# Kernel tuning notes

Measured on AMD Instinct MI355X. Metric: run time of the kernel, lower is better.

## Reference

```python
import jax, jax.numpy as jnp
import numpy as np

B, S, D, I, L, H, F = 4, 512, 768, 64, 2, 12, 3072
DH = D // H
LN_EPS = 1e-12


def setup_inputs() -> dict:
    key = jax.random.key(0)
    ks = jax.random.split(key, 24)
    nrm = lambda k, sh, s=0.02: jax.random.normal(k, sh, jnp.float32) * s
    return {
        'hs0': nrm(ks[0], (B, S, D), 1.0),
        'hs1': nrm(ks[1], (B, S, D), 1.0),
        'hs2': nrm(ks[2], (B, S, D), 1.0),
        'Wq': nrm(ks[3], (L, D, D)), 'bq': jnp.zeros((L, D), jnp.float32),
        'Wk': nrm(ks[4], (L, D, D)), 'bk': jnp.zeros((L, D), jnp.float32),
        'Wv': nrm(ks[5], (L, D, D)), 'bv': jnp.zeros((L, D), jnp.float32),
        'Wo': nrm(ks[6], (L, D, D)), 'bo': jnp.zeros((L, D), jnp.float32),
        'ln1_g': jnp.ones((L, D), jnp.float32), 'ln1_b': jnp.zeros((L, D), jnp.float32),
        'W1': nrm(ks[7], (L, D, F)), 'b1': jnp.zeros((L, F), jnp.float32),
        'W2': nrm(ks[8], (L, F, D)), 'b2': jnp.zeros((L, D), jnp.float32),
        'ln2_g': jnp.ones((L, D), jnp.float32), 'ln2_b': jnp.zeros((L, D), jnp.float32),
        'zero_context': nrm(ks[9], (D,), 1.0),
        'ck2tok_mask': jax.random.uniform(ks[10], (B, I, S)) > 0.7,  # True = token excluded from span
        'span_size_ids': jax.random.randint(ks[11], (B, I), 0, 10),
    }


def _ln(x, g, b):
    m = jnp.mean(x, axis=-1, keepdims=True)
    v = jnp.mean((x - m) ** 2, axis=-1, keepdims=True)
    return (x - m) * jax.lax.rsqrt(v + LN_EPS) * g + b


def _forward(hs0, hs1, Wq, bq, Wk, bk, Wv, bv, Wo, bo, ln1_g, ln1_b,
             W1, b1, W2, b2, ln2_g, ln2_b, zero_context, mask):
    # mask: [B,I,S] bool, True = excluded token
    zero_indic = jnp.all(mask, axis=-1)                 # [B,I] spans with no valid token
    mask = mask & ~zero_indic[:, :, None]               # unmask degenerate rows (replaced at end)
    # masked max pooling (init aggregation) -- [B,I,S,D] intermediate, traffic-bound
    pooled = jnp.max(jnp.where(mask[..., None], -jnp.inf, hs0[:, None, :, :]), axis=2)  # [B,I,D]
    ext = (mask.astype(jnp.float32) * -10000.0)[:, None, :, :]  # [B,1,I,S] extended attn mask
    q = pooled
    hs_list = (hs0, hs1)
    inv_sqrt_dh = np.float32(1.0 / np.sqrt(DH))
    for i in range(L):
        hs = hs_list[i]
        qh = (q @ Wq[i] + bq[i]).reshape(B, I, H, DH).transpose(0, 2, 1, 3)   # [B,H,I,DH]
        kh = (hs @ Wk[i] + bk[i]).reshape(B, S, H, DH).transpose(0, 2, 1, 3)  # [B,H,S,DH]
        vh = (hs @ Wv[i] + bv[i]).reshape(B, S, H, DH).transpose(0, 2, 1, 3)
        scores = jnp.einsum('bhid,bhsd->bhis', qh, kh) * inv_sqrt_dh + ext
        attn = jax.nn.softmax(scores, axis=-1)
        ctx = jnp.einsum('bhis,bhsd->bhid', attn, vh).transpose(0, 2, 1, 3).reshape(B, I, D)
        q = _ln(q + ctx @ Wo[i] + bo[i], ln1_g[i], ln1_b[i])
        ffn = jax.nn.gelu(q @ W1[i] + b1[i], approximate=False) @ W2[i] + b2[i]
        q = _ln(q + ffn, ln2_g[i], ln2_b[i])
    # zero-context substitution for empty spans
    return jnp.where(zero_indic[..., None], zero_context, q)


def reference(hs0, hs1, hs2, Wq, bq, Wk, bk, Wv, bv, Wo, bo, ln1_g, ln1_b,
              W1, b1, W2, b2, ln2_g, ln2_b, zero_context, ck2tok_mask, span_size_ids):
    # hs2 is the last entry of the (num_layers+1) slice; query layers 0..L-1 attend hs0..hs1.
    # span_size_ids unused since use_init_size_emb=False.
    del hs2, span_size_ids
    return _forward(hs0, hs1, Wq, bq, Wk, bk, Wv, bv, Wo, bo, ln1_g, ln1_b,
                    W1, b1, W2, b2, ln2_g, ln2_b, zero_context, ck2tok_mask)
```

## Files before the change

kernel.cpp:

```cpp
#include <hip/hip_runtime.h>
#include <hip/hip_bf16.h>
#include <math.h>

#define BB 4
#define SS 512
#define DD 768
#define II 64
#define LL 2
#define HH 12
#define FF 3072

using short8 = __attribute__((ext_vector_type(8))) short;
using f32x4  = __attribute__((ext_vector_type(4))) float;

__device__ __forceinline__ unsigned short f2bf(float x) {
  return __builtin_bit_cast(unsigned short, __float2bfloat16(x));
}

__device__ __forceinline__ void gload_lds16(const void* g, void* l) {
  __builtin_amdgcn_global_load_lds((const __attribute__((address_space(1))) unsigned int*)g,
                                   (__attribute__((address_space(3))) unsigned int*)l, 16, 0, 0);
}

struct TC { const float* s[6]; };

__global__ __launch_bounds__(256) void prep_kernel(
    TC src, unsigned short* __restrict__ WT4, unsigned short* __restrict__ W1T,
    unsigned short* __restrict__ W2T,
    const float* __restrict__ hs0, const float* __restrict__ hs1,
    unsigned short* __restrict__ hsb0, unsigned short* __restrict__ hsb1,
    const int* __restrict__ mask, int* __restrict__ zi, float* __restrict__ qf,
    unsigned short* __restrict__ qb, unsigned long long* __restrict__ pmask) {
  __shared__ float smem[4096];
  int id = blockIdx.x;
  int t = threadIdx.x;
  if (id < 3456) {
    const float* Ws; unsigned short* WTs; int K, N, k0, n0;
    if (id < 1152) {
      int z = id / 144, rem = id - z * 144;
      int widx = z >> 1, l = z & 1;
      Ws = src.s[widx] + (size_t)l * DD * DD;
      WTs = WT4 + ((size_t)widx * 2 + l) * DD * DD;
      K = DD; N = DD; k0 = (rem / 6) * 32; n0 = (rem % 6) * 128;
    } else if (id < 2304) {
      int j = id - 1152, l = j / 576, rem = j - l * 576;
      Ws = src.s[4] + (size_t)l * DD * FF;
      WTs = W1T + (size_t)l * FF * DD;
      K = DD; N = FF; k0 = (rem / 24) * 32; n0 = (rem % 24) * 128;
    } else {
      int j = id - 2304, l = j / 576, rem = j - l * 576;
      Ws = src.s[5] + (size_t)l * FF * DD;
      WTs = W2T + (size_t)l * DD * FF;
      K = FF; N = DD; k0 = (rem / 6) * 32; n0 = (rem % 6) * 128;
    }
    int w = t >> 6, lane = t & 63;
    #pragma unroll
    for (int cc = 0; cc < 4; ++cc) {
      int c = w * 4 + cc;
      int row = c * 2 + (lane >> 5);
      int cbyte = (lane & 31) * 16;
      int scb = cbyte ^ ((row & 7) << 4);
      gload_lds16((const char*)(Ws + (size_t)(k0 + row) * N + n0) + scb,
                  (char*)smem + c * 1024);
    }
    __syncthreads();
    int n = t >> 1, h2 = t & 1;
    union { unsigned short u[16]; uint4 v4[2]; } pk;
    #pragma unroll
    for (int i = 0; i < 16; ++i) {
      int kl = h2 * 16 + i;
      float f = *(const float*)((const char*)smem + kl * 512 + ((n * 4) ^ ((kl & 7) << 4)));
      pk.u[i] = f2bf(f);
    }
    uint4* dst = (uint4*)(WTs + (size_t)(n0 + n) * K + k0 + h2 * 16);
    dst[0] = pk.v4[0];
    dst[1] = pk.v4[1];
  } else if (id < 4992) {
    int idx = (id - 3456) * 256 + t;
    float4 va = ((const float4*)hs0)[idx];
    float4 vb = ((const float4*)hs1)[idx];
    union { unsigned short u[4]; uint2 v; } pa, pb;
    pa.u[0] = f2bf(va.x); pa.u[1] = f2bf(va.y); pa.u[2] = f2bf(va.z); pa.u[3] = f2bf(va.w);
    pb.u[0] = f2bf(vb.x); pb.u[1] = f2bf(vb.y); pb.u[2] = f2bf(vb.z); pb.u[3] = f2bf(vb.w);
    ((uint2*)hsb0)[idx] = pa.v;
    ((uint2*)hsb1)[idx] = pb.v;
  } else {
    float* eadd = smem;
    int j = id - 4992;
    int bi = j & 255, dz = j >> 8;
    int b = bi >> 6, w = t >> 6;
    const int* mrow = mask + (size_t)bi * SS;
    int m0v = mrow[t], m1v = mrow[t + 256];
    eadd[t] = m0v ? -__builtin_inff() : 0.0f;
    eadd[t + 256] = m1v ? -__builtin_inff() : 0.0f;
    int incl = (m0v == 0) | (m1v == 0);
    int any = __syncthreads_or(incl);
    int z = !any;
    if (dz == 0) {
      unsigned long long w0 = __ballot(z || (m0v == 0));
      unsigned long long w1 = __ballot(z || (m1v == 0));
      if ((t & 63) == 0) {
        pmask[bi * 8 + w] = w0;
        pmask[bi * 8 + 4 + w] = w1;
        if (t == 0) zi[bi] = z;
      }
    }
    const float* hb = hs0 + (size_t)b * SS * DD + dz * 256 + t;
    float m[8];
    #pragma unroll
    for (int jj = 0; jj < 8; ++jj) m[jj] = -3.4e38f;
    for (int s0 = 0; s0 < SS; s0 += 8) {
      #pragma unroll
      for (int jj = 0; jj < 8; ++jj)
        m[jj] = fmaxf(m[jj], hb[(size_t)(s0 + jj) * DD] + eadd[s0 + jj]);
    }
    float mm = fmaxf(fmaxf(fmaxf(m[0], m[1]), fmaxf(m[2], m[3])),
                     fmaxf(fmaxf(m[4], m[5]), fmaxf(m[6], m[7])));
    size_t o = (size_t)bi * DD + dz * 256 + t;
    qf[o] = mm;
    qb[o] = f2bf(mm);
  }
}

struct GB { const unsigned short* A; const unsigned short* Bt; const float* bias; void* C;
            int M; int N; int rowbias; };

template <int GELU, int OUTBF>
__global__ __launch_bounds__(256) void gemm_nt(GB g0, GB g1, GB g2, GB g3, int K) {
  __shared__ unsigned short Al[2][128 * 64];
  __shared__ unsigned short Bl[2][128 * 64];
  GB g = (blockIdx.z == 0) ? g0 : (blockIdx.z == 1) ? g1 : (blockIdx.z == 2) ? g2 : g3;
  int bm = blockIdx.x, bn = blockIdx.y;
  if (blockIdx.z & 1) { bm = blockIdx.y; bn = blockIdx.x; }
  if (bm * 128 >= g.M) return;
  int t = threadIdx.x, w = t >> 6, lane = t & 63;
  int hi = lane >> 4, lo = lane & 15;
  int wr = w >> 1, wc = w & 1;
  f32x4 acc[4][4] = {};
  const char* Abase = (const char*)g.A + (size_t)(bm * 128) * (size_t)K * 2;
  const char* Bbase = (const char*)g.Bt + (size_t)(bn * 128) * (size_t)K * 2;
  int rowbytes = K * 2;
  int KT = K >> 6;
  auto STAGE = [&](int buf, int kt) {
    int k0b = kt * 128;
    #pragma unroll
    for (int c = 0; c < 4; ++c) {
      int base = (c * 4 + w) << 10;
      int o = base + lane * 16;
      int row = o >> 7, cb = o & 127;
      int scb = cb ^ ((row & 7) << 4);
      gload_lds16(Abase + (size_t)row * rowbytes + (k0b + scb), (char*)Al[buf] + base);
      gload_lds16(Bbase + (size_t)row * rowbytes + (k0b + scb), (char*)Bl[buf] + base);
    }
  };
  STAGE(0, 0);
  asm volatile("s_waitcnt vmcnt(0)" ::: "memory");
  __builtin_amdgcn_s_barrier();
  int cur = 0;
  for (int kt = 0; kt < KT; ++kt) {
    if (kt + 1 < KT) STAGE(cur ^ 1, kt + 1);
    #pragma unroll
    for (int kk = 0; kk < 2; ++kk) {
      short8 av[4], bv_[4];
      #pragma unroll
      for (int mi = 0; mi < 4; ++mi) {
        int r = wr * 64 + mi * 16 + lo;
        av[mi] = *(const short8*)((const char*)Al[cur] + r * 128 + ((kk * 64 + hi * 16) ^ ((r & 7) << 4)));
      }
      #pragma unroll
      for (int ni = 0; ni < 4; ++ni) {
        int r = wc * 64 + ni * 16 + lo;
        bv_[ni] = *(const short8*)((const char*)Bl[cur] + r * 128 + ((kk * 64 + hi * 16) ^ ((r & 7) << 4)));
      }
      #pragma unroll
      for (int mi = 0; mi < 4; ++mi)
        #pragma unroll
        for (int ni = 0; ni < 4; ++ni)
          acc[mi][ni] = __builtin_amdgcn_mfma_f32_16x16x32_bf16(av[mi], bv_[ni], acc[mi][ni], 0, 0, 0);
    }
    if (kt + 1 < KT) {
      asm volatile("s_waitcnt vmcnt(0)" ::: "memory");
      __builtin_amdgcn_s_barrier();
      cur ^= 1;
    }
  }
  int mbase = bm * 128 + wr * 64;
  int nbase = bn * 128 + wc * 64;
  #pragma unroll
  for (int mi = 0; mi < 4; ++mi)
    #pragma unroll
    for (int ni = 0; ni < 4; ++ni)
      #pragma unroll
      for (int r = 0; r < 4; ++r) {
        int gm = mbase + mi * 16 + hi * 4 + r;
        int gn = nbase + ni * 16 + lo;
        float v = acc[mi][ni][r] + (g.rowbias ? g.bias[gm] : g.bias[gn]);
        if (GELU) v = 0.5f * v * (1.0f + erff(v * 0.70710678118654752f));
        if (OUTBF) ((unsigned short*)g.C)[(size_t)gm * g.N + gn] = f2bf(v);
        else       ((float*)g.C)[(size_t)gm * g.N + gn] = v;
      }
}

template <int GELU, int OUTBF, int PARTIAL>
__global__ __launch_bounds__(256) void gemm_sk(GB g, int K, int kLen) {
  __shared__ unsigned short Al[2][64 * 64];
  __shared__ unsigned short Bl[2][64 * 64];
  int bm = blockIdx.x, bn = blockIdx.y, bz = blockIdx.z;
  int t = threadIdx.x, w = t >> 6, lane = t & 63;
  int hi = lane >> 4, lo = lane & 15;
  int wr = w >> 1, wc = w & 1;
  f32x4 acc[2][2] = {};
  size_t rb = (size_t)K * 2;
  const char* Abase = (const char*)g.A + (size_t)(bm * 64) * rb + (size_t)bz * kLen * 2;
  const char* Bbase = (const char*)g.Bt + (size_t)(bn * 64) * rb + (size_t)bz * kLen * 2;
  int KT = kLen >> 6;
  auto STAGE = [&](int buf, int kt) {
    int k0b = kt * 128;
    #pragma unroll
    for (int c = 0; c < 2; ++c) {
      int base = (c * 4 + w) << 10;
      int o = base + lane * 16;
      int row = o >> 7, cb = o & 127;
      int scb = cb ^ ((row & 7) << 4);
      gload_lds16(Abase + (size_t)row * rb + (k0b + scb), (char*)Al[buf] + base);
      gload_lds16(Bbase + (size_t)row * rb + (k0b + scb), (char*)Bl[buf] + base);
    }
  };
  STAGE(0, 0);
  asm volatile("s_waitcnt vmcnt(0)" ::: "memory");
  __builtin_amdgcn_s_barrier();
  int cur = 0;
  for (int kt = 0; kt < KT; ++kt) {
    if (kt + 1 < KT) STAGE(cur ^ 1, kt + 1);
    #pragma unroll
    for (int kk = 0; kk < 2; ++kk) {
      short8 av[2], bv_[2];
      #pragma unroll
      for (int mi = 0; mi < 2; ++mi) {
        int r = wr * 32 + mi * 16 + lo;
        av[mi] = *(const short8*)((const char*)Al[cur] + r * 128 + ((kk * 64 + hi * 16) ^ ((r & 7) << 4)));
      }
      #pragma unroll
      for (int ni = 0; ni < 2; ++ni) {
        int r = wc * 32 + ni * 16 + lo;
        bv_[ni] = *(const short8*)((const char*)Bl[cur] + r * 128 + ((kk * 64 + hi * 16) ^ ((r & 7) << 4)));
      }
      #pragma unroll
      for (int mi = 0; mi < 2; ++mi)
        #pragma unroll
        for (int ni = 0; ni < 2; ++ni)
          acc[mi][ni] = __builtin_amdgcn_mfma_f32_16x16x32_bf16(av[mi], bv_[ni], acc[mi][ni], 0, 0, 0);
    }
    if (kt + 1 < KT) {
      asm volatile("s_waitcnt vmcnt(0)" ::: "memory");
      __builtin_amdgcn_s_barrier();
      cur ^= 1;
    }
  }
  int mbase = bm * 64 + wr * 32;
  int nbase = bn * 64 + wc * 32;
  #pragma unroll
  for (int mi = 0; mi < 2; ++mi)
    #pragma unroll
    for (int ni = 0; ni < 2; ++ni)
      #pragma unroll
      for (int r = 0; r < 4; ++r) {
        int gm = mbase + mi * 16 + hi * 4 + r;
        int gn = nbase + ni * 16 + lo;
        if (PARTIAL) {
          ((float*)g.C)[((size_t)bz * g.M + gm) * g.N + gn] = acc[mi][ni][r];
        } else {
          float v = acc[mi][ni][r] + g.bias[gn];
          if (GELU) v = 0.5f * v * (1.0f + erff(v * 0.70710678118654752f));
          if (OUTBF) ((unsigned short*)g.C)[(size_t)gm * g.N + gn] = f2bf(v);
          else       ((float*)g.C)[(size_t)gm * g.N + gn] = v;
        }
      }
}

#define ATTN_LDS 145664
__global__ __launch_bounds__(256) void attn_kernel(
    const unsigned short* __restrict__ qbuf, const unsigned short* __restrict__ WqTl,
    const float* __restrict__ bql, const unsigned short* __restrict__ khb,
    const unsigned short* __restrict__ vTall, const unsigned long long* __restrict__ pmask,
    unsigned short* __restrict__ ctx) {
  extern __shared__ char lds[];
  char* Qd = lds;
  char* KP = lds + 8192;
  char* Vd = lds + 8192 + 65536;
  unsigned long long* pm = (unsigned long long*)(lds + 139264);
  float* red  = (float*)(lds + 143360);
  float* red2 = (float*)(lds + 144384);
  float* rnv  = (float*)(lds + 145408);
  int bh = blockIdx.x;
  int b = bh / HH, h = bh - b * HH;
  int t = threadIdx.x, w = t >> 6, l = t & 63, hi = l >> 4, lo = l & 15;
  int o16 = l * 16, ro = o16 >> 7, cb = o16 & 127;

  const char* vsrc = (const char*)vTall + (size_t)(h * 64) * 4096 + (size_t)b * 1024;
  #pragma unroll
  for (int rr = 0; rr < 16; ++rr) {
    int rv = w * 16 + rr;
    gload_lds16(vsrc + (size_t)rv * 4096 + ((l * 16) ^ ((rv & 7) << 4)), Vd + rv * 1024);
  }
  if (w == 0) {
    const char* psrc = (const char*)pmask + (size_t)b * 4096;
    #pragma unroll
    for (int c = 0; c < 4; ++c) gload_lds16(psrc + c * 1024 + l * 16, (char*)pm + c * 1024);
  }

  const char* Aq = (const char*)qbuf + (size_t)(b * II) * 1536;
  const char* Bq = (const char*)WqTl + (size_t)(h * 64) * 1536;
  f32x4 qacc[4] = {};
  #pragma unroll
  for (int cc = 0; cc < 2; ++cc) {
    int ch = w * 2 + cc, row = ch * 8 + ro;
    int scb = cb ^ ((row & 7) << 4);
    gload_lds16(Aq + (size_t)row * 1536 + scb, KP + ch * 1024);
    gload_lds16(Bq + (size_t)row * 1536 + scb, KP + 8192 + ch * 1024);
  }
  __syncthreads();
  for (int kt = 0; kt < 12; ++kt) {
    int cur = (kt & 1) * 16384;
    if (kt < 11) {
      int nxt = ((kt + 1) & 1) * 16384;
      int kb = (kt + 1) * 128;
      #pragma unroll
      for (int cc = 0; cc < 2; ++cc) {
        int ch = w * 2 + cc, row = ch * 8 + ro;
        int scb = kb + (cb ^ ((row & 7) << 4));
        gload_lds16(Aq + (size_t)row * 1536 + scb, KP + nxt + ch * 1024);
        gload_lds16(Bq + (size_t)row * 1536 + scb, KP + nxt + 8192 + ch * 1024);
      }
    }
    #pragma unroll
    for (int kk = 0; kk < 2; ++kk) {
      int ra = w * 16 + lo;
      short8 av = *(const short8*)(KP + cur + ra * 128 + ((kk * 64 + hi * 16) ^ ((ra & 7) << 4)));
      #pragma unroll
      for (int ni = 0; ni < 4; ++ni) {
        int rb2 = ni * 16 + lo;
        short8 bv = *(const short8*)(KP + cur + 8192 + rb2 * 128 + ((kk * 64 + hi * 16) ^ ((rb2 & 7) << 4)));
        qacc[ni] = __builtin_amdgcn_mfma_f32_16x16x32_bf16(av, bv, qacc[ni], 0, 0, 0);
      }
    }
    __syncthreads();
  }
  #pragma unroll
  for (int ni = 0; ni < 4; ++ni)
    #pragma unroll
    for (int r = 0; r < 4; ++r) {
      int row = w * 16 + hi * 4 + r, col = ni * 16 + lo;
      float v = qacc[ni][r] + bql[h * 64 + col];
      *(unsigned short*)(Qd + row * 128 + ((col * 2) ^ ((row & 7) << 4))) = f2bf(v);
    }
  const char* Ks = (const char*)khb + (size_t)(b * SS) * 1536 + h * 128;
  #pragma unroll
  for (int cc = 0; cc < 16; ++cc) {
    int ch = w * 16 + cc, row = ch * 8 + ro;
    int scb = cb ^ ((row & 7) << 4);
    gload_lds16(Ks + (size_t)row * 1536 + scb, KP + ch * 1024);
  }
  __syncthreads();

  f32x4 acc[4][8] = {};
  #pragma unroll
  for (int kk = 0; kk < 2; ++kk) {
    short8 av[4];
    #pragma unroll
    for (int mi = 0; mi < 4; ++mi) {
      int ra = mi * 16 + lo;
      av[mi] = *(const short8*)(Qd + ra * 128 + ((kk * 64 + hi * 16) ^ ((ra & 7) << 4)));
    }
    #pragma unroll
    for (int ni = 0; ni < 8; ++ni) {
      int rk = w * 128 + ni * 16 + lo;
      short8 bv = *(const short8*)(KP + rk * 128 + ((kk * 64 + hi * 16) ^ ((rk & 7) << 4)));
      #pragma unroll
      for (int mi = 0; mi < 4; ++mi)
        acc[mi][ni] = __builtin_amdgcn_mfma_f32_16x16x32_bf16(av[mi], bv, acc[mi][ni], 0, 0, 0);
    }
  }
  #pragma unroll
  for (int mi = 0; mi < 4; ++mi)
    #pragma unroll
    for (int r = 0; r < 4; ++r) {
      float m = acc[mi][0][r];
      #pragma unroll
      for (int ni = 1; ni < 8; ++ni) m = fmaxf(m, acc[mi][ni][r]);
      #pragma unroll
      for (int xm = 1; xm <= 8; xm <<= 1) m = fmaxf(m, __shfl_xor(m, xm));
      if (lo == 0) red[(mi * 16 + hi * 4 + r) * 4 + w] = m;
    }
  __syncthreads();
  #pragma unroll
  for (int mi = 0; mi < 4; ++mi)
    #pragma unroll
    for (int r = 0; r < 4; ++r) {
      int row = mi * 16 + hi * 4 + r;
      float4 rm4 = *(const float4*)&red[row * 4];
      float gm = fmaxf(fmaxf(rm4.x, rm4.y), fmaxf(rm4.z, rm4.w));
      unsigned long long w0 = pm[row * 8 + w * 2 + 0];
      unsigned long long w1 = pm[row * 8 + w * 2 + 1];
      float s = 0.f;
      #pragma unroll
      for (int ni = 0; ni < 8; ++ni) {
        int sl = ni * 16 + lo;
        unsigned long long word = (sl < 64) ? w0 : w1;
        float in = ((word >> (sl & 63)) & 1ull) ? 1.0f : 0.0f;
        float e = __expf((acc[mi][ni][r] - gm) * 0.125f) * in;
        s += e;
        int sbyte = w * 256 + ni * 32 + lo * 2;
        *(unsigned short*)(KP + row * 1024 + (sbyte ^ ((row & 7) << 4))) = f2bf(e);
      }
      #pragma unroll
      for (int xm = 1; xm <= 8; xm <<= 1) s += __shfl_xor(s, xm);
      if (lo == 0) red2[row * 4 + w] = s;
    }
  __syncthreads();
  if (w == 0 && lo == 0) {
    #pragma unroll
    for (int mi = 0; mi < 4; ++mi)
      #pragma unroll
      for (int r = 0; r < 4; ++r) {
        int row = mi * 16 + hi * 4 + r;
        float4 s4 = *(const float4*)&red2[row * 4];
        rnv[row] = 1.0f / ((s4.x + s4.y) + (s4.z + s4.w));
      }
  }
  __syncthreads();
  f32x4 pacc[4] = {};
  for (int kk = 0; kk < 16; ++kk) {
    int rv = w * 16 + lo;
    short8 bv = *(const short8*)(Vd + rv * 1024 + ((kk * 64 + hi * 16) ^ ((rv & 7) << 4)));
    #pragma unroll
    for (int mi = 0; mi < 4; ++mi) {
      int ra = mi * 16 + lo;
      short8 av = *(const short8*)(KP + ra * 1024 + ((kk * 64 + hi * 16) ^ ((ra & 7) << 4)));
      pacc[mi] = __builtin_amdgcn_mfma_f32_16x16x32_bf16(av, bv, pacc[mi], 0, 0, 0);
    }
  }
  #pragma unroll
  for (int mi = 0; mi < 4; ++mi)
    #pragma unroll
    for (int r = 0; r < 4; ++r) {
      int row = mi * 16 + hi * 4 + r;
      ctx[(size_t)(b * II + row) * DD + h * 64 + w * 16 + lo] = f2bf(pacc[mi][r] * rnv[row]);
    }
}

template <int FINAL, int NP>
__global__ __launch_bounds__(256) void ln_kernel(const float* __restrict__ x, const float* __restrict__ y,
                                                 const float* __restrict__ gb,
                                                 const float* __restrict__ g, const float* __restrict__ bb,
                                                 float* __restrict__ qf, unsigned short* __restrict__ qb,
                                                 const int* __restrict__ zi, const float* __restrict__ zc,
                                                 float* __restrict__ out) {
  __shared__ float r1[4], r2[4];
  const int MN = BB * II * DD;
  int r = blockIdx.x, t = threadIdx.x;
  size_t o = (size_t)r * DD;
  float v0 = x[o + t] + gb[t];
  float v1 = x[o + t + 256] + gb[t + 256];
  float v2 = x[o + t + 512] + gb[t + 512];
  #pragma unroll
  for (int p = 0; p < NP; ++p) {
    size_t po = (size_t)p * MN + o;
    v0 += y[po + t];
    v1 += y[po + t + 256];
    v2 += y[po + t + 512];
  }
  float s = v0 + v1 + v2, ss = v0 * v0 + v1 * v1 + v2 * v2;
  #pragma unroll
  for (int o2 = 32; o2; o2 >>= 1) { s += __shfl_xor(s, o2); ss += __shfl_xor(ss, o2); }
  if ((t & 63) == 0) { r1[t >> 6] = s; r2[t >> 6] = ss; }
  __syncthreads();
  s = r1[0] + r1[1] + r1[2] + r1[3];
  ss = r2[0] + r2[1] + r2[2] + r2[3];
  float mean = s * (1.0f / DD);
  float var = ss * (1.0f / DD) - mean * mean;
  float inv = rsqrtf(var + 1e-12f);
  float w0 = (v0 - mean) * inv * g[t] + bb[t];
  float w1 = (v1 - mean) * inv * g[t + 256] + bb[t + 256];
  float w2 = (v2 - mean) * inv * g[t + 512] + bb[t + 512];
  if (FINAL) {
    int z = zi[r];
    out[o + t] = z ? zc[t] : w0;
    out[o + t + 256] = z ? zc[t + 256] : w1;
    out[o + t + 512] = z ? zc[t + 512] : w2;
  } else {
    qf[o + t] = w0; qf[o + t + 256] = w1; qf[o + t + 512] = w2;
    qb[o + t] = f2bf(w0); qb[o + t + 256] = f2bf(w1); qb[o + t + 512] = f2bf(w2);
  }
}

extern "C" void kernel_launch(void* const* d_in, const int* in_sizes, int n_in,
                              void* d_out, int out_size, void* d_ws, size_t ws_size,
                              hipStream_t stream) {
  (void)in_sizes; (void)n_in; (void)out_size; (void)ws_size;
  const float* hs0 = (const float*)d_in[0];
  const float* hs1 = (const float*)d_in[1];
  const float* Wq  = (const float*)d_in[3];
  const float* bq  = (const float*)d_in[4];
  const float* Wk  = (const float*)d_in[5];
  const float* bk  = (const float*)d_in[6];
  const float* Wv  = (const float*)d_in[7];
  const float* bv  = (const float*)d_in[8];
  const float* Wo  = (const float*)d_in[9];
  const float* bo  = (const float*)d_in[10];
  const float* ln1g = (const float*)d_in[11];
  const float* ln1b = (const float*)d_in[12];
  const float* W1  = (const float*)d_in[13];
  const float* b1  = (const float*)d_in[14];
  const float* W2  = (const float*)d_in[15];
  const float* b2  = (const float*)d_in[16];
  const float* ln2g = (const float*)d_in[17];
  const float* ln2b = (const float*)d_in[18];
  const float* zc  = (const float*)d_in[19];
  const int*   mask = (const int*)d_in[20];

  char* ws = (char*)d_ws;
  size_t off = 0;
  auto alloc = [&](size_t bytes) { size_t o = off; off += (bytes + 255) & ~(size_t)255; return o; };

  unsigned short* WT4 = (unsigned short*)(ws + alloc((size_t)4 * LL * DD * DD * 2));
  unsigned short* W1T = (unsigned short*)(ws + alloc((size_t)LL * FF * DD * 2));
  unsigned short* W2T = (unsigned short*)(ws + alloc((size_t)LL * DD * FF * 2));
  unsigned short* hsb = (unsigned short*)(ws + alloc((size_t)2 * BB * SS * DD * 2));
  float*          qf  = (float*)(ws + alloc((size_t)BB * II * DD * 4));
  unsigned short* qb  = (unsigned short*)(ws + alloc((size_t)BB * II * DD * 2));
  unsigned short* khb = (unsigned short*)(ws + alloc((size_t)LL * BB * SS * DD * 2));
  unsigned short* vTall = (unsigned short*)(ws + alloc((size_t)LL * DD * BB * SS * 2));
  unsigned short* ctxb = (unsigned short*)(ws + alloc((size_t)BB * II * DD * 2));
  float*          att_o = (float*)(ws + alloc((size_t)2 * BB * II * DD * 4));
  unsigned short* ffh = (unsigned short*)(ws + alloc((size_t)BB * II * FF * 2));
  float*          ffo = (float*)(ws + alloc((size_t)4 * BB * II * DD * 4));
  unsigned long long* pmask = (unsigned long long*)(ws + alloc((size_t)BB * II * 8 * 8));
  int*            zib = (int*)(ws + alloc((size_t)BB * II * 4));

  unsigned short* WqT = WT4 + 0 * (size_t)LL * DD * DD;
  unsigned short* WkT = WT4 + 1 * (size_t)LL * DD * DD;
  unsigned short* WvT = WT4 + 2 * (size_t)LL * DD * DD;
  unsigned short* WoT = WT4 + 3 * (size_t)LL * DD * DD;

  (void)hipFuncSetAttribute((const void*)attn_kernel,
                            hipFuncAttributeMaxDynamicSharedMemorySize, ATTN_LDS);

  TC tc = { { Wq, Wk, Wv, Wo, W1, W2 } };
  prep_kernel<<<5760, 256, 0, stream>>>(tc, WT4, W1T, W2T, hs0, hs1,
                                        hsb, hsb + (size_t)BB * SS * DD,
                                        mask, zib, qf, qb, pmask);

  {
    const unsigned short* h0 = hsb;
    const unsigned short* h1 = hsb + (size_t)BB * SS * DD;
    GB gK0 = { h0, WkT, bk, khb, BB * SS, DD, 0 };
    GB gV0 = { WvT, h0, bv, vTall, DD, BB * SS, 1 };
    GB gK1 = { h1, WkT + (size_t)DD * DD, bk + DD, khb + (size_t)BB * SS * DD, BB * SS, DD, 0 };
    GB gV1 = { WvT + (size_t)DD * DD, h1, bv + DD, vTall + (size_t)DD * BB * SS, DD, BB * SS, 1 };
    gemm_nt<0, 1><<<dim3(16, 6, 4), 256, 0, stream>>>(gK0, gV0, gK1, gV1, DD);
  }

  for (int l = 0; l < LL; ++l) {
    const unsigned short* khl = khb + (size_t)l * BB * SS * DD;
    const unsigned short* vTl = vTall + (size_t)l * DD * BB * SS;
    attn_kernel<<<dim3(BB * HH), 256, ATTN_LDS, stream>>>(
        qb, WqT + (size_t)l * DD * DD, bq + l * DD, khl, vTl, pmask, ctxb);
    GB gO = { ctxb, WoT + (size_t)l * DD * DD, nullptr, att_o, BB * II, DD, 0 };
    gemm_sk<0, 0, 1><<<dim3(4, 12, 2), 256, 0, stream>>>(gO, DD, DD / 2);
    ln_kernel<0, 2><<<BB * II, 256, 0, stream>>>(qf, att_o, bo + l * DD,
                                                 ln1g + l * DD, ln1b + l * DD, qf, qb,
                                                 nullptr, nullptr, nullptr);
    GB gF1 = { qb, W1T + (size_t)l * FF * DD, b1 + l * FF, ffh, BB * II, FF, 0 };
    gemm_sk<1, 1, 0><<<dim3(4, FF / 64, 1), 256, 0, stream>>>(gF1, DD, DD);
    GB gF2 = { ffh, W2T + (size_t)l * DD * FF, nullptr, ffo, BB * II, DD, 0 };
    gemm_sk<0, 0, 1><<<dim3(4, 12, 4), 256, 0, stream>>>(gF2, FF, FF / 4);
    if (l == 0)
      ln_kernel<0, 4><<<BB * II, 256, 0, stream>>>(qf, ffo, b2 + l * DD,
                                                   ln2g + l * DD, ln2b + l * DD, qf, qb,
                                                   nullptr, nullptr, nullptr);
    else
      ln_kernel<1, 4><<<BB * II, 256, 0, stream>>>(qf, ffo, b2 + l * DD,
                                                   ln2g + l * DD, ln2b + l * DD, nullptr, nullptr,
                                                   zib, zc, (float*)d_out);
  }
}
```

Before: 183.3 us.

## Split prep kernel and reuse staged hidden-state tiles across four spans in pooling

The monolithic prep kernel is split into three kernels: a cast+mask kernel that also writes a byte exclusion mask, a weight transpose-cast kernel with 64-deep k tiles (fewer, larger blocks), and a new pooling kernel. The pooling kernel stages hs0 chunks into LDS with double-buffered async loads and has each block compute the max for four spans at once. The old path reread hs0 from global memory separately for every span. The change adds two kernel launches and a new byte-mask buffer, and the pooling grid is only 192 blocks, so the GPU may be underfilled.

```diff
diff --git a/kernel.cpp b/kernel.cpp
--- a/kernel.cpp
+++ b/kernel.cpp
@@ -22,61 +22,14 @@
                                    (__attribute__((address_space(3))) unsigned int*)l, 16, 0, 0);
 }
 
-struct TC { const float* s[6]; };
-
-__global__ __launch_bounds__(256) void prep_kernel(
-    TC src, unsigned short* __restrict__ WT4, unsigned short* __restrict__ W1T,
-    unsigned short* __restrict__ W2T,
+__global__ __launch_bounds__(256) void castmask_kernel(
     const float* __restrict__ hs0, const float* __restrict__ hs1,
     unsigned short* __restrict__ hsb0, unsigned short* __restrict__ hsb1,
-    const int* __restrict__ mask, int* __restrict__ zi, float* __restrict__ qf,
-    unsigned short* __restrict__ qb, unsigned long long* __restrict__ pmask) {
-  __shared__ float smem[4096];
-  int id = blockIdx.x;
-  int t = threadIdx.x;
-  if (id < 3456) {
-    const float* Ws; unsigned short* WTs; int K, N, k0, n0;
-    if (id < 1152) {
-      int z = id / 144, rem = id - z * 144;
-      int widx = z >> 1, l = z & 1;
-      Ws = src.s[widx] + (size_t)l * DD * DD;
-      WTs = WT4 + ((size_t)widx * 2 + l) * DD * DD;
-      K = DD; N = DD; k0 = (rem / 6) * 32; n0 = (rem % 6) * 128;
-    } else if (id < 2304) {
-      int j = id - 1152, l = j / 576, rem = j - l * 576;
-      Ws = src.s[4] + (size_t)l * DD * FF;
-      WTs = W1T + (size_t)l * FF * DD;
-      K = DD; N = FF; k0 = (rem / 24) * 32; n0 = (rem % 24) * 128;
-    } else {
-      int j = id - 2304, l = j / 576, rem = j - l * 576;
-      Ws = src.s[5] + (size_t)l * FF * DD;
-      WTs = W2T + (size_t)l * DD * FF;
-      K = FF; N = DD; k0 = (rem / 6) * 32; n0 = (rem % 6) * 128;
-    }
-    int w = t >> 6, lane = t & 63;
-    #pragma unroll
-    for (int cc = 0; cc < 4; ++cc) {
-      int c = w * 4 + cc;
-      int row = c * 2 + (lane >> 5);
-      int cbyte = (lane & 31) * 16;
-      int scb = cbyte ^ ((row & 7) << 4);
-      gload_lds16((const char*)(Ws + (size_t)(k0 + row) * N + n0) + scb,
-                  (char*)smem + c * 1024);
-    }
-    __syncthreads();
-    int n = t >> 1, h2 = t & 1;
-    union { unsigned short u[16]; uint4 v4[2]; } pk;
-    #pragma unroll
-    for (int i = 0; i < 16; ++i) {
-      int kl = h2 * 16 + i;
-      float f = *(const float*)((const char*)smem + kl * 512 + ((n * 4) ^ ((kl & 7) << 4)));
-      pk.u[i] = f2bf(f);
-    }
-    uint4* dst = (uint4*)(WTs + (size_t)(n0 + n) * K + k0 + h2 * 16);
-    dst[0] = pk.v4[0];
-    dst[1] = pk.v4[1];
-  } else if (id < 4992) {
-    int idx = (id - 3456) * 256 + t;
+    const int* __restrict__ mask, int* __restrict__ zi,
+    unsigned long long* __restrict__ pmask, unsigned char* __restrict__ emask) {
+  int id = blockIdx.x, t = threadIdx.x;
+  if (id < 1536) {
+    int idx = id * 256 + t;
     float4 va = ((const float4*)hs0)[idx];
     float4 vb = ((const float4*)hs1)[idx];
     union { unsigned short u[4]; uint2 v; } pa, pb;
@@ -85,41 +38,130 @@
     ((uint2*)hsb0)[idx] = pa.v;
     ((uint2*)hsb1)[idx] = pb.v;
   } else {
-    float* eadd = smem;
-    int j = id - 4992;
-    int bi = j & 255, dz = j >> 8;
-    int b = bi >> 6, w = t >> 6;
+    int bi = id - 1536;
+    int w = t >> 6;
     const int* mrow = mask + (size_t)bi * SS;
     int m0v = mrow[t], m1v = mrow[t + 256];
-    eadd[t] = m0v ? -__builtin_inff() : 0.0f;
-    eadd[t + 256] = m1v ? -__builtin_inff() : 0.0f;
     int incl = (m0v == 0) | (m1v == 0);
     int any = __syncthreads_or(incl);
     int z = !any;
-    if (dz == 0) {
-      unsigned long long w0 = __ballot(z || (m0v == 0));
-      unsigned long long w1 = __ballot(z || (m1v == 0));
-      if ((t & 63) == 0) {
-        pmask[bi * 8 + w] = w0;
-        pmask[bi * 8 + 4 + w] = w1;
-        if (t == 0) zi[bi] = z;
-      }
-    }
-    const float* hb = hs0 + (size_t)b * SS * DD + dz * 256 + t;
-    float m[8];
-    #pragma unroll
-    for (int jj = 0; jj < 8; ++jj) m[jj] = -3.4e38f;
-    for (int s0 = 0; s0 < SS; s0 += 8) {
-      #pragma unroll
-      for (int jj = 0; jj < 8; ++jj)
-        m[jj] = fmaxf(m[jj], hb[(size_t)(s0 + jj) * DD] + eadd[s0 + jj]);
-    }
-    float mm = fmaxf(fmaxf(fmaxf(m[0], m[1]), fmaxf(m[2], m[3])),
-                     fmaxf(fmaxf(m[4], m[5]), fmaxf(m[6], m[7])));
-    size_t o = (size_t)bi * DD + dz * 256 + t;
-    qf[o] = mm;
-    qb[o] = f2bf(mm);
-  }
+    unsigned long long w0 = __ballot(z || (m0v == 0));
+    unsigned long long w1 = __ballot(z || (m1v == 0));
+    if ((t & 63) == 0) {
+      pmask[bi * 8 + w] = w0;
+      pmask[bi * 8 + 4 + w] = w1;
+      if (t == 0) zi[bi] = z;
+    }
+    emask[(size_t)bi * SS + t] = (unsigned char)((!z) & (m0v != 0));
+    emask[(size_t)bi * SS + t + 256] = (unsigned char)((!z) & (m1v != 0));
+  }
+}
+
+struct TC { const float* s[6]; };
+
+__global__ __launch_bounds__(256) void tcast_kernel(TC src, unsigned short* __restrict__ WT4,
+                                                    unsigned short* __restrict__ W1T,
+                                                    unsigned short* __restrict__ W2T) {
+  __shared__ float smem[8192];
+  int id = blockIdx.x, t = threadIdx.x;
+  const float* Ws; unsigned short* WTs; int K, N, k0, n0;
+  if (id < 576) {
+    int z = id / 72, rem = id - z * 72;
+    int widx = z >> 1, l = z & 1;
+    Ws = src.s[widx] + (size_t)l * DD * DD;
+    WTs = WT4 + ((size_t)widx * 2 + l) * DD * DD;
+    K = DD; N = DD; k0 = (rem / 6) * 64; n0 = (rem % 6) * 128;
+  } else if (id < 1152) {
+    int j = id - 576, l = j / 288, rem = j - l * 288;
+    Ws = src.s[4] + (size_t)l * DD * FF;
+    WTs = W1T + (size_t)l * FF * DD;
+    K = DD; N = FF; k0 = (rem / 24) * 64; n0 = (rem % 24) * 128;
+  } else {
+    int j = id - 1152, l = j / 288, rem = j - l * 288;
+    Ws = src.s[5] + (size_t)l * FF * DD;
+    WTs = W2T + (size_t)l * DD * FF;
+    K = FF; N = DD; k0 = (rem / 6) * 64; n0 = (rem % 6) * 128;
+  }
+  int w = t >> 6, lane = t & 63;
+  #pragma unroll
+  for (int cc = 0; cc < 8; ++cc) {
+    int c = w * 8 + cc;
+    int row = c * 2 + (lane >> 5);
+    int cbyte = (lane & 31) * 16;
+    int scb = cbyte ^ ((row & 7) << 4);
+    gload_lds16((const char*)(Ws + (size_t)(k0 + row) * N + n0) + scb, (char*)smem + c * 1024);
+  }
+  __syncthreads();
+  int n = t >> 1, kh = t & 1;
+  union { unsigned short u[32]; uint4 v4[4]; } pk;
+  #pragma unroll
+  for (int i = 0; i < 32; ++i) {
+    int kl = kh * 32 + i;
+    float f = *(const float*)((const char*)smem + kl * 512 + ((n * 4) ^ ((kl & 7) << 4)));
+    pk.u[i] = f2bf(f);
+  }
+  uint4* dst = (uint4*)(WTs + (size_t)(n0 + n) * K + k0 + kh * 32);
+  dst[0] = pk.v4[0]; dst[1] = pk.v4[1]; dst[2] = pk.v4[2]; dst[3] = pk.v4[3];
+}
+
+#define PCH 32
+__global__ __launch_bounds__(256) void pool2_kernel(const float* __restrict__ hs0,
+                                                    const unsigned char* __restrict__ emask,
+                                                    float* __restrict__ qf,
+                                                    unsigned short* __restrict__ qb) {
+  __shared__ float hsb[2][PCH * 256];
+  __shared__ unsigned char em[4 * SS];
+  int id = blockIdx.x;
+  int ig = id & 15, bdz = id >> 4;
+  int dz = bdz % 3, b = bdz / 3;
+  int t = threadIdx.x, w = t >> 6, lane = t & 63;
+  if (w == 0) {
+    const char* esrc = (const char*)emask + ((size_t)(b * II + ig * 4)) * SS;
+    gload_lds16(esrc + lane * 16, (char*)em);
+    gload_lds16(esrc + 1024 + lane * 16, (char*)em + 1024);
+  }
+  const float* hb = hs0 + (size_t)(b * SS) * DD + dz * 256;
+  auto STAGE = [&](int buf, int it) {
+    #pragma unroll
+    for (int cc = 0; cc < 8; ++cc) {
+      int c = w * 8 + cc;
+      gload_lds16((const char*)(hb + (size_t)(it * PCH + c) * DD) + lane * 16,
+                  (char*)hsb[buf] + c * 1024);
+    }
+  };
+  STAGE(0, 0);
+  float m0 = -3.4e38f, m1 = -3.4e38f, m2 = -3.4e38f, m3 = -3.4e38f;
+  const float NEG = -__builtin_inff();
+  int cur = 0;
+  for (int it = 0; it < 16; ++it) {
+    if (it + 1 < 16) {
+      STAGE(cur ^ 1, it + 1);
+      asm volatile("s_waitcnt vmcnt(8)" ::: "memory");
+    } else {
+      asm volatile("s_waitcnt vmcnt(0)" ::: "memory");
+    }
+    __builtin_amdgcn_s_barrier();
+    const float* hp = hsb[cur];
+    const unsigned char* e0 = em + it * PCH;
+    const unsigned char* e1 = e0 + SS;
+    const unsigned char* e2 = e1 + SS;
+    const unsigned char* e3 = e2 + SS;
+    #pragma unroll 8
+    for (int s = 0; s < PCH; ++s) {
+      float v = hp[s * 256 + t];
+      m0 = fmaxf(m0, v + (e0[s] ? NEG : 0.0f));
+      m1 = fmaxf(m1, v + (e1[s] ? NEG : 0.0f));
+      m2 = fmaxf(m2, v + (e2[s] ? NEG : 0.0f));
+      m3 = fmaxf(m3, v + (e3[s] ? NEG : 0.0f));
+    }
+    __builtin_amdgcn_s_barrier();
+    cur ^= 1;
+  }
+  size_t r0 = (size_t)(b * II + ig * 4) * DD + dz * 256 + t;
+  qf[r0] = m0;          qb[r0] = f2bf(m0);
+  qf[r0 + DD] = m1;     qb[r0 + DD] = f2bf(m1);
+  qf[r0 + 2 * DD] = m2; qb[r0 + 2 * DD] = f2bf(m2);
+  qf[r0 + 3 * DD] = m3; qb[r0 + 3 * DD] = f2bf(m3);
 }
 
 struct GB { const unsigned short* A; const unsigned short* Bt; const float* bias; void* C;
@@ -536,6 +578,7 @@
   unsigned short* ffh = (unsigned short*)(ws + alloc((size_t)BB * II * FF * 2));
   float*          ffo = (float*)(ws + alloc((size_t)4 * BB * II * DD * 4));
   unsigned long long* pmask = (unsigned long long*)(ws + alloc((size_t)BB * II * 8 * 8));
+  unsigned char*  emask = (unsigned char*)(ws + alloc((size_t)BB * II * SS));
   int*            zib = (int*)(ws + alloc((size_t)BB * II * 4));
 
   unsigned short* WqT = WT4 + 0 * (size_t)LL * DD * DD;
@@ -546,10 +589,11 @@
   (void)hipFuncSetAttribute((const void*)attn_kernel,
                             hipFuncAttributeMaxDynamicSharedMemorySize, ATTN_LDS);
 
+  castmask_kernel<<<1536 + 256, 256, 0, stream>>>(hs0, hs1, hsb, hsb + (size_t)BB * SS * DD,
+                                                  mask, zib, pmask, emask);
   TC tc = { { Wq, Wk, Wv, Wo, W1, W2 } };
-  prep_kernel<<<5760, 256, 0, stream>>>(tc, WT4, W1T, W2T, hs0, hs1,
-                                        hsb, hsb + (size_t)BB * SS * DD,
-                                        mask, zib, qf, qb, pmask);
+  tcast_kernel<<<1728, 256, 0, stream>>>(tc, WT4, W1T, W2T);
+  pool2_kernel<<<192, 256, 0, stream>>>(hs0, emask, qf, qb);
 
   {
     const unsigned short* h0 = hsb;
```

After: 199.2 us. 1.09x slower.
